# Kernel tuning notes

Measured on AMD Instinct MI355X. Metric: run time of the kernel, lower is better.

The kernel has to match this reference:

```python
import jax, jax.numpy as jnp
import numpy as np

HID = 128  # hidden_channel
C = 256    # feat_channel

def conv1x1(x, w, b):
    # x: [N, Cin, H, W], w: [Cout, Cin], b: [Cout]
    return jnp.einsum('nchw,oc->nohw', x, w) + b[None, :, None, None]

def maxpool2(x):
    N, Ch, H, W = x.shape
    return x.reshape(N, Ch, H // 2, 2, W // 2, 2).max(axis=(3, 5))

def setup_inputs() -> dict:
    key = jax.random.key(0)
    ks = jax.random.split(key, 6)
    rois = jax.random.normal(ks[0], (128, C, 14, 14), dtype=jnp.float32)
    feature = jax.random.normal(ks[1], (2, C, 64, 64), dtype=jnp.float32)
    s_in = 1.0 / np.sqrt(C)
    s_hid = 1.0 / np.sqrt(HID)
    wq = jax.random.uniform(ks[2], (HID, C), minval=-s_in, maxval=s_in, dtype=jnp.float32)
    wk = jax.random.uniform(ks[3], (HID, C), minval=-s_in, maxval=s_in, dtype=jnp.float32)
    wv = jax.random.uniform(ks[4], (HID, C), minval=-s_in, maxval=s_in, dtype=jnp.float32)
    wre = jax.random.uniform(ks[5], (C, HID), minval=-s_hid, maxval=s_hid, dtype=jnp.float32)
    return {
        'rois': rois, 'feature': feature,
        'wq': wq, 'bq': jnp.zeros((HID,), jnp.float32),
        'wk': wk, 'bk': jnp.zeros((HID,), jnp.float32),
        'wv': wv, 'bv': jnp.zeros((HID,), jnp.float32),
        'wre': wre, 'bre': jnp.zeros((C,), jnp.float32),
    }

def reference(rois, feature, wq, bq, wk, bk, wv, bv, wre, bre):
    BS_roinum, Cf, h, w = rois.shape
    BS = feature.shape[0]
    roinum = BS_roinum // BS
    _h, _w = h // 2, w // 2

    # Q at full resolution
    q = conv1x1(rois, wq, bq)                              # [BS*R, HID, h, w]
    q = q.transpose(0, 2, 3, 1).reshape(BS, roinum * h * w, HID)

    ds = maxpool2(rois)                                    # [BS*R, C, _h, _w]
    k = conv1x1(ds, wk, bk).transpose(0, 2, 3, 1).reshape(BS, roinum * _h * _w, HID)
    v = conv1x1(ds, wv, bv).transpose(0, 2, 3, 1).reshape(BS, roinum * _h * _w, HID)

    score = jnp.einsum('bqc,bkc->bqk', q, k)               # [BS, R*h*w, R*_h*_w]
    score = jax.nn.softmax(score, axis=-1)
    y = jnp.einsum('bqk,bkc->bqc', score, v)               # [BS, R*h*w, HID]

    y = y.reshape(BS * roinum, h, w, HID).transpose(0, 3, 1, 2)
    y = conv1x1(y, wre, bre)                               # [BS*R, C, h, w]
    return rois + y
```

## Files before the change

### kernel.cpp

```cpp
#include <hip/hip_runtime.h>
#include <math.h>

constexpr int CIN  = 256;
constexpr int HID  = 128;
constexpr int P    = 196;
constexpr int PP   = 49;
constexpr int NQ   = 12544;
constexpr int NKEY = 3136;

using f32x4 = __attribute__((ext_vector_type(4))) float;
using s16x8 = __attribute__((ext_vector_type(8))) short;
using s16x4 = __attribute__((ext_vector_type(4))) short;
using u32x2 = __attribute__((ext_vector_type(2))) unsigned int;

__device__ __forceinline__ unsigned short f2bf(float x) {
    unsigned int u = __float_as_uint(x);
    u += 0x7FFFu + ((u >> 16) & 1u);
    return (unsigned short)(u >> 16);
}
__device__ __forceinline__ float bf2f(unsigned short s) {
    return __uint_as_float(((unsigned int)s) << 16);
}

__global__ __launch_bounds__(256) void prep_kernel(
    const float* __restrict__ rois,
    const float* __restrict__ wq, const float* __restrict__ wk,
    const float* __restrict__ wv, const float* __restrict__ wre,
    unsigned short* __restrict__ xq, unsigned short* __restrict__ xkv,
    unsigned short* __restrict__ wqb, unsigned short* __restrict__ wkb,
    unsigned short* __restrict__ wvb, unsigned short* __restrict__ wreb)
{
    const int bx = blockIdx.x;
    const int t  = threadIdx.x;

    if (bx >= 512) {
        const int which = bx - 512;
        const float* src = (which == 0) ? wq : (which == 1) ? wk : (which == 2) ? wv : wre;
        unsigned short* dst = (which == 0) ? wqb : (which == 1) ? wkb
                             : (which == 2) ? wvb : wreb;
        #pragma unroll 4
        for (int i = 0; i < 32; ++i) {
            const int idx = i * 256 + t;
            const float4 v = ((const float4*)src)[idx];
            s16x4 o;
            o[0] = (short)f2bf(v.x); o[1] = (short)f2bf(v.y);
            o[2] = (short)f2bf(v.z); o[3] = (short)f2bf(v.w);
            *(s16x4*)(dst + idx * 4) = o;
        }
        return;
    }

    const int n = bx >> 2;
    const int g = bx & 3;
    const int b = n >> 6, r = n & 63;
    __shared__ float xT[196 * 68];

    const int c_loc = t >> 2;
    const int pq    = t & 3;

    const float4* row4 = (const float4*)(rois + ((size_t)n * CIN + g * 64 + c_loc) * P);
    #pragma unroll
    for (int j = 0; j < 13; ++j) {
        const int idx4 = pq + 4 * j;
        if (idx4 < 49) {
            const float4 v = row4[idx4];
            xT[(idx4 * 4 + 0) * 68 + c_loc] = v.x;
            xT[(idx4 * 4 + 1) * 68 + c_loc] = v.y;
            xT[(idx4 * 4 + 2) * 68 + c_loc] = v.z;
            xT[(idx4 * 4 + 3) * 68 + c_loc] = v.w;
        }
    }
    __syncthreads();

    #pragma unroll
    for (int i = 0; i < 7; ++i) {
        const int u = i * 256 + t;
        if (u < 1568) {
            const int px = u >> 3, ch8 = (u & 7) * 8;
            s16x8 o;
            #pragma unroll
            for (int e = 0; e < 8; ++e)
                o[e] = (short)f2bf(xT[px * 68 + ch8 + e]);
            *(s16x8*)(xq + ((size_t)b * NQ + r * P + px) * CIN + g * 64 + ch8) = o;
        }
    }
    #pragma unroll
    for (int i = 0; i < 2; ++i) {
        const int u = i * 256 + t;
        if (u < 392) {
            const int pp = u >> 3, ch8 = (u & 7) * 8;
            const int py = pp / 7, px_ = pp - py * 7;
            const int base00 = (py * 2) * 14 + px_ * 2;
            s16x8 o;
            #pragma unroll
            for (int e = 0; e < 8; ++e) {
                const int c = ch8 + e;
                const float m0 = fmaxf(xT[(base00)      * 68 + c], xT[(base00 + 1)  * 68 + c]);
                const float m1 = fmaxf(xT[(base00 + 14) * 68 + c], xT[(base00 + 15) * 68 + c]);
                o[e] = (short)f2bf(fmaxf(m0, m1));
            }
            *(s16x8*)(xkv + ((size_t)b * NKEY + r * PP + pp) * CIN + g * 64 + ch8) = o;
        }
    }
}

__global__ __launch_bounds__(256) void gemm_fused_kernel(
    const unsigned short* __restrict__ xq, const unsigned short* __restrict__ xkv,
    const unsigned short* __restrict__ wqb, const unsigned short* __restrict__ wkb,
    const unsigned short* __restrict__ wvb,
    const float* __restrict__ bq, const float* __restrict__ bk, const float* __restrict__ bv,
    unsigned short* __restrict__ q, unsigned short* __restrict__ kmat,
    unsigned short* __restrict__ vt_g)
{
    const int bx = blockIdx.x;
    const unsigned short* x; const unsigned short* w; const float* bias;
    int m_blk, mode;
    if (bx < 196)      { mode = 0; x = xq;  w = wqb; bias = bq; m_blk = bx; }
    else if (bx < 245) { mode = 1; x = xkv; w = wkb; bias = bk; m_blk = bx - 196; }
    else               { mode = 2; x = xkv; w = wvb; bias = bv; m_blk = bx - 245; }

    const int t = threadIdx.x;
    const int wid = t >> 6, lane = t & 63;
    const int quad = lane >> 4, c = lane & 15;
    const int m_base = m_blk * 128 + (wid & 1) * 64;
    const int n_base = (wid >> 1) * 64;

    f32x4 acc[4][4];
    #pragma unroll
    for (int i = 0; i < 4; ++i)
        #pragma unroll
        for (int j = 0; j < 4; ++j) acc[i][j] = (f32x4)(0.f);

    #pragma unroll
    for (int ks = 0; ks < 8; ++ks) {
        s16x8 af[4], bf[4];
        #pragma unroll
        for (int mt = 0; mt < 4; ++mt)
            af[mt] = *(const s16x8*)(x + (size_t)(m_base + mt * 16 + c) * CIN + ks * 32 + quad * 8);
        #pragma unroll
        for (int nt = 0; nt < 4; ++nt)
            bf[nt] = *(const s16x8*)(w + (size_t)(n_base + nt * 16 + c) * CIN + ks * 32 + quad * 8);
        #pragma unroll
        for (int mt = 0; mt < 4; ++mt)
            #pragma unroll
            for (int nt = 0; nt < 4; ++nt)
                acc[mt][nt] = __builtin_amdgcn_mfma_f32_16x16x32_bf16(af[mt], bf[nt], acc[mt][nt], 0, 0, 0);
    }

    if (mode <= 1) {
        unsigned short* out = (mode == 0) ? q : kmat;
        #pragma unroll
        for (int nt = 0; nt < 4; ++nt) {
            const float bv_ = bias[n_base + nt * 16 + c];
            #pragma unroll
            for (int mt = 0; mt < 4; ++mt)
                #pragma unroll
                for (int rr = 0; rr < 4; ++rr) {
                    const int m = m_base + mt * 16 + quad * 4 + rr;
                    out[(size_t)m * HID + n_base + nt * 16 + c] = f2bf(acc[mt][nt][rr] + bv_);
                }
        }
    } else {
        #pragma unroll
        for (int nt = 0; nt < 4; ++nt) {
            const int d = n_base + nt * 16 + c;
            const float bv_ = bias[d];
            #pragma unroll
            for (int mt = 0; mt < 4; ++mt)
                #pragma unroll
                for (int rr = 0; rr < 4; ++rr) {
                    const int key_g = m_base + mt * 16 + quad * 4 + rr;
                    const int bb = (key_g >= NKEY) ? 1 : 0;
                    const int kl = key_g - bb * NKEY;
                    vt_g[((size_t)bb * HID + d) * NKEY + kl] = f2bf(acc[mt][nt][rr] + bv_);
                }
        }
    }
}

__global__ __launch_bounds__(128, 2) void attn_kernel(
    const unsigned short* __restrict__ q, const unsigned short* __restrict__ kmat,
    const unsigned short* __restrict__ vt_g,
    unsigned short* __restrict__ opart, float* __restrict__ lpart)
{
    const int b    = blockIdx.y;
    const int s    = blockIdx.z;
    const int tid  = threadIdx.x;
    const int w    = tid >> 6;
    const int lane = tid & 63;
    const int quad = lane >> 4;
    const int c    = lane & 15;
    const int qb   = blockIdx.x * 128 + w * 64;

    __shared__ unsigned short Ps[2][64 * 72];

    const unsigned short* qg = q    + (size_t)b * NQ   * HID;
    const unsigned short* kg = kmat + (size_t)b * NKEY * HID;
    const unsigned short* vt = vt_g + (size_t)b * HID  * NKEY;

    s16x8 qf[4][4];
    #pragma unroll
    for (int nt = 0; nt < 4; ++nt)
        #pragma unroll
        for (int ks = 0; ks < 4; ++ks)
            qf[nt][ks] = *(const s16x8*)(qg + (size_t)(qb + nt * 16 + c) * HID + ks * 32 + quad * 8);

    f32x4 Ob[4][8];
    #pragma unroll
    for (int nt = 0; nt < 4; ++nt)
        #pragma unroll
        for (int nd = 0; nd < 8; ++nd) Ob[nt][nd] = (f32x4)(0.f);
    float l[4] = {0.f, 0.f, 0.f, 0.f};

    const int B6[6] = {0, 20, 40, 60, 79, 98};
    const int kt0 = B6[s], kt1 = B6[s + 1];

    for (int kt = kt0; kt < kt1; ++kt) {
        const int kb = kt * 32;

        f32x4 st[2][4];
        #pragma unroll
        for (int mt = 0; mt < 2; ++mt)
            #pragma unroll
            for (int nt = 0; nt < 4; ++nt) st[mt][nt] = (f32x4)(0.f);
        #pragma unroll
        for (int mt = 0; mt < 2; ++mt) {
            s16x8 kf[4];
            #pragma unroll
            for (int ks = 0; ks < 4; ++ks)
                kf[ks] = *(const s16x8*)(kg + (size_t)(kb + mt * 16 + c) * HID + ks * 32 + quad * 8);
            #pragma unroll
            for (int ks = 0; ks < 4; ++ks)
                #pragma unroll
                for (int nt = 0; nt < 4; ++nt)
                    st[mt][nt] = __builtin_amdgcn_mfma_f32_16x16x32_bf16(kf[ks], qf[nt][ks], st[mt][nt], 0, 0, 0);
        }

        #pragma unroll
        for (int mt = 0; mt < 2; ++mt) {
            #pragma unroll
            for (int nt = 0; nt < 4; ++nt) {
                const float e0 = __expf(st[mt][nt][0]);
                const float e1 = __expf(st[mt][nt][1]);
                const float e2 = __expf(st[mt][nt][2]);
                const float e3 = __expf(st[mt][nt][3]);
                l[nt] += (e0 + e1) + (e2 + e3);
                u32x2 pk;
                pk[0] = (unsigned int)f2bf(e0) | ((unsigned int)f2bf(e1) << 16);
                pk[1] = (unsigned int)f2bf(e2) | ((unsigned int)f2bf(e3) << 16);
                *(u32x2*)&Ps[w][(nt * 16 + c) * 72 + mt * 16 + quad * 4] = pk;
            }
        }

        s16x8 pf[4];
        #pragma unroll
        for (int nt = 0; nt < 4; ++nt)
            pf[nt] = *(const s16x8*)&Ps[w][(nt * 16 + c) * 72 + quad * 8];
        #pragma unroll
        for (int g2 = 0; g2 < 2; ++g2) {
            s16x8 vf[4];
            #pragma unroll
            for (int dd = 0; dd < 4; ++dd)
                vf[dd] = *(const s16x8*)(vt + (size_t)((g2 * 4 + dd) * 16 + c) * NKEY + kb + quad * 8);
            #pragma unroll
            for (int dd = 0; dd < 4; ++dd)
                #pragma unroll
                for (int nt = 0; nt < 4; ++nt)
                    Ob[nt][g2 * 4 + dd] = __builtin_amdgcn_mfma_f32_16x16x32_bf16(pf[nt], vf[dd], Ob[nt][g2 * 4 + dd], 0, 0, 0);
        }
    }

    unsigned short* Op = opart + (size_t)(s * 2 + b) * NQ * HID;
    #pragma unroll
    for (int nt = 0; nt < 4; ++nt) {
        #pragma unroll
        for (int nd = 0; nd < 8; ++nd) {
            #pragma unroll
            for (int rr = 0; rr < 4; ++rr) {
                const int qrow = qb + nt * 16 + quad * 4 + rr;
                Op[(size_t)qrow * HID + nd * 16 + c] = f2bf(Ob[nt][nd][rr]);
            }
        }
    }
    #pragma unroll
    for (int nt = 0; nt < 4; ++nt) {
        l[nt] += __shfl_xor(l[nt], 16, 64);
        l[nt] += __shfl_xor(l[nt], 32, 64);
    }
    if (quad == 0) {
        float* lp = lpart + (size_t)(s * 2 + b) * NQ;
        #pragma unroll
        for (int nt = 0; nt < 4; ++nt) lp[qb + nt * 16 + c] = l[nt];
    }
}

__global__ __launch_bounds__(256) void outproj_kernel(
    const float* __restrict__ rois,
    const unsigned short* __restrict__ opart, const float* __restrict__ lpart,
    const unsigned short* __restrict__ wreb, const float* __restrict__ bre,
    float* __restrict__ out)
{
    const int t = threadIdx.x;
    const int wid = t >> 6, lane = t & 63;
    const int quad = lane >> 4, c = lane & 15;
    const int m0 = blockIdx.x * 64;
    const int b  = (m0 >= NQ) ? 1 : 0;

    __shared__ unsigned short ys[64 * 136];

    {
        const int m_loc = t >> 2, kq = t & 3;
        const int q_local = (m0 + m_loc) - b * NQ;
        float lsum = 0.f;
        #pragma unroll
        for (int sl = 0; sl < 5; ++sl)
            lsum += lpart[(size_t)(sl * 2 + b) * NQ + q_local];
        const float invl = 1.0f / lsum;
        #pragma unroll
        for (int ch = 0; ch < 4; ++ch) {
            float a8[8] = {0, 0, 0, 0, 0, 0, 0, 0};
            #pragma unroll
            for (int sl = 0; sl < 5; ++sl) {
                const s16x8 v = *(const s16x8*)&opart[
                    ((size_t)(sl * 2 + b) * NQ + q_local) * HID + kq * 32 + ch * 8];
                #pragma unroll
                for (int e = 0; e < 8; ++e) a8[e] += bf2f((unsigned short)v[e]);
            }
            s16x8 o;
            #pragma unroll
            for (int e = 0; e < 8; ++e) o[e] = (short)f2bf(a8[e] * invl);
            *(s16x8*)&ys[m_loc * 136 + kq * 32 + ch * 8] = o;
        }
    }
    __syncthreads();

    const int o_base = wid * 64;
    s16x8 af[4][4];
    #pragma unroll
    for (int mt = 0; mt < 4; ++mt)
        #pragma unroll
        for (int ks = 0; ks < 4; ++ks)
            af[mt][ks] = *(const s16x8*)(wreb + (size_t)(o_base + mt * 16 + c) * HID + ks * 32 + quad * 8);

    f32x4 acc[4][4];
    #pragma unroll
    for (int i = 0; i < 4; ++i)
        #pragma unroll
        for (int j = 0; j < 4; ++j) acc[i][j] = (f32x4)(0.f);

    #pragma unroll
    for (int ks = 0; ks < 4; ++ks) {
        s16x8 bf[4];
        #pragma unroll
        for (int nt = 0; nt < 4; ++nt)
            bf[nt] = *(const s16x8*)&ys[(nt * 16 + c) * 136 + ks * 32 + quad * 8];
        #pragma unroll
        for (int mt = 0; mt < 4; ++mt)
            #pragma unroll
            for (int nt = 0; nt < 4; ++nt)
                acc[mt][nt] = __builtin_amdgcn_mfma_f32_16x16x32_bf16(af[mt][ks], bf[nt], acc[mt][nt], 0, 0, 0);
    }

    #pragma unroll
    for (int nt = 0; nt < 4; ++nt) {
        const int m_g = m0 + nt * 16 + c;
        const int mm  = m_g - b * NQ;
        const int r_roi = mm / 196;
        const int p     = mm - r_roi * 196;
        const int n_img = b * 64 + r_roi;
        const size_t base = ((size_t)n_img * CIN) * P + p;
        #pragma unroll
        for (int mt = 0; mt < 4; ++mt) {
            #pragma unroll
            for (int rr = 0; rr < 4; ++rr) {
                const int o = o_base + mt * 16 + quad * 4 + rr;
                out[base + (size_t)o * P] = rois[base + (size_t)o * P] + bre[o] + acc[mt][nt][rr];
            }
        }
    }
}

extern "C" void kernel_launch(void* const* d_in, const int* in_sizes, int n_in,
                              void* d_out, int out_size, void* d_ws, size_t ws_size,
                              hipStream_t stream)
{
    (void)in_sizes; (void)n_in; (void)out_size; (void)ws_size;
    const float* rois = (const float*)d_in[0];
    const float* wq  = (const float*)d_in[2];
    const float* bq  = (const float*)d_in[3];
    const float* wk  = (const float*)d_in[4];
    const float* bk  = (const float*)d_in[5];
    const float* wv  = (const float*)d_in[6];
    const float* bv  = (const float*)d_in[7];
    const float* wre = (const float*)d_in[8];
    const float* bre = (const float*)d_in[9];
    float* out = (float*)d_out;

    char* ws = (char*)d_ws;
    unsigned short* opart = (unsigned short*)(ws);
    unsigned short* xq    = (unsigned short*)(ws);
    unsigned short* xkv   = (unsigned short*)(ws + 12845056);
    unsigned short* wqb   = (unsigned short*)(ws + 16056320);
    unsigned short* wkb   = (unsigned short*)(ws + 16121856);
    unsigned short* wvb   = (unsigned short*)(ws + 16187392);
    unsigned short* q     = (unsigned short*)(ws + 32112640);
    unsigned short* kmat  = (unsigned short*)(ws + 38535168);
    unsigned short* vt_g  = (unsigned short*)(ws + 40140800);
    float*          lpart = (float*)         (ws + 41746432);
    unsigned short* wreb  = (unsigned short*)(ws + 42248192);

    prep_kernel<<<dim3(516), 256, 0, stream>>>(rois, wq, wk, wv, wre,
                                               xq, xkv, wqb, wkb, wvb, wreb);
    gemm_fused_kernel<<<dim3(294), 256, 0, stream>>>(xq, xkv, wqb, wkb, wvb,
                                                     bq, bk, bv, q, kmat, vt_g);
    attn_kernel<<<dim3(98, 2, 5), 128, 0, stream>>>(q, kmat, vt_g, opart, lpart);
    outproj_kernel<<<dim3(392), 256, 0, stream>>>(rois, opart, lpart, wreb, bre, out);
}
```

Baseline: 230.1 us.

## Make attention key-split count depend on workspace size; use cheaper bf16 packing

Attention split count S over the key dimension now depends on the available workspace (10, 8 or 5), which raises the grid size and the occupancy of the attention kernel. The workspace layout is recomputed so each split gets its own partial-output buffer, and the reduce loop in outproj is generalized to S. Separately, the bf16 conversion changes from round-to-nearest-even to a simpler round-half-up and packs pairs with v_perm, so it uses fewer instructions. The trade-off is more partial-sum traffic in the reduce, and slightly different rounding.

Result: slower. 240.4 us (+4.5%).

```diff
diff --git a/kernel.cpp b/kernel.cpp
--- a/kernel.cpp
+++ b/kernel.cpp
@@ -12,11 +12,15 @@
 using s16x8 = __attribute__((ext_vector_type(8))) short;
 using s16x4 = __attribute__((ext_vector_type(4))) short;
 using u32x2 = __attribute__((ext_vector_type(2))) unsigned int;
+using u32x4 = __attribute__((ext_vector_type(4))) unsigned int;
 
 __device__ __forceinline__ unsigned short f2bf(float x) {
-    unsigned int u = __float_as_uint(x);
-    u += 0x7FFFu + ((u >> 16) & 1u);
-    return (unsigned short)(u >> 16);
+    return (unsigned short)((__float_as_uint(x) + 0x8000u) >> 16);
+}
+__device__ __forceinline__ unsigned int pack_bf16(float a, float b) {
+    const unsigned int ua = __float_as_uint(a) + 0x8000u;
+    const unsigned int ub = __float_as_uint(b) + 0x8000u;
+    return __builtin_amdgcn_perm(ua, ub, 0x03020706u);
 }
 __device__ __forceinline__ float bf2f(unsigned short s) {
     return __uint_as_float(((unsigned int)s) << 16);
@@ -42,10 +46,10 @@
         for (int i = 0; i < 32; ++i) {
             const int idx = i * 256 + t;
             const float4 v = ((const float4*)src)[idx];
-            s16x4 o;
-            o[0] = (short)f2bf(v.x); o[1] = (short)f2bf(v.y);
-            o[2] = (short)f2bf(v.z); o[3] = (short)f2bf(v.w);
-            *(s16x4*)(dst + idx * 4) = o;
+            u32x2 o;
+            o[0] = pack_bf16(v.x, v.y);
+            o[1] = pack_bf16(v.z, v.w);
+            *(u32x2*)(dst + idx * 4) = o;
         }
         return;
     }
@@ -77,11 +81,11 @@
         const int u = i * 256 + t;
         if (u < 1568) {
             const int px = u >> 3, ch8 = (u & 7) * 8;
-            s16x8 o;
-            #pragma unroll
-            for (int e = 0; e < 8; ++e)
-                o[e] = (short)f2bf(xT[px * 68 + ch8 + e]);
-            *(s16x8*)(xq + ((size_t)b * NQ + r * P + px) * CIN + g * 64 + ch8) = o;
+            u32x4 o;
+            #pragma unroll
+            for (int e = 0; e < 4; ++e)
+                o[e] = pack_bf16(xT[px * 68 + ch8 + 2 * e], xT[px * 68 + ch8 + 2 * e + 1]);
+            *(u32x4*)(xq + ((size_t)b * NQ + r * P + px) * CIN + g * 64 + ch8) = o;
         }
     }
     #pragma unroll
@@ -91,15 +95,18 @@
             const int pp = u >> 3, ch8 = (u & 7) * 8;
             const int py = pp / 7, px_ = pp - py * 7;
             const int base00 = (py * 2) * 14 + px_ * 2;
-            s16x8 o;
+            float mx[8];
             #pragma unroll
             for (int e = 0; e < 8; ++e) {
                 const int c = ch8 + e;
                 const float m0 = fmaxf(xT[(base00)      * 68 + c], xT[(base00 + 1)  * 68 + c]);
                 const float m1 = fmaxf(xT[(base00 + 14) * 68 + c], xT[(base00 + 15) * 68 + c]);
-                o[e] = (short)f2bf(fmaxf(m0, m1));
+                mx[e] = fmaxf(m0, m1);
             }
-            *(s16x8*)(xkv + ((size_t)b * NKEY + r * PP + pp) * CIN + g * 64 + ch8) = o;
+            u32x4 o;
+            #pragma unroll
+            for (int e = 0; e < 4; ++e) o[e] = pack_bf16(mx[2 * e], mx[2 * e + 1]);
+            *(u32x4*)(xkv + ((size_t)b * NKEY + r * PP + pp) * CIN + g * 64 + ch8) = o;
         }
     }
 }
@@ -181,7 +188,7 @@
 __global__ __launch_bounds__(128, 2) void attn_kernel(
     const unsigned short* __restrict__ q, const unsigned short* __restrict__ kmat,
     const unsigned short* __restrict__ vt_g,
-    unsigned short* __restrict__ opart, float* __restrict__ lpart)
+    unsigned short* __restrict__ opart, float* __restrict__ lpart, int S)
 {
     const int b    = blockIdx.y;
     const int s    = blockIdx.z;
@@ -212,8 +219,8 @@
         for (int nd = 0; nd < 8; ++nd) Ob[nt][nd] = (f32x4)(0.f);
     float l[4] = {0.f, 0.f, 0.f, 0.f};
 
-    const int B6[6] = {0, 20, 40, 60, 79, 98};
-    const int kt0 = B6[s], kt1 = B6[s + 1];
+    const int kt0 = (98 * s) / S;
+    const int kt1 = (98 * (s + 1)) / S;
 
     for (int kt = kt0; kt < kt1; ++kt) {
         const int kb = kt * 32;
@@ -246,8 +253,8 @@
                 const float e3 = __expf(st[mt][nt][3]);
                 l[nt] += (e0 + e1) + (e2 + e3);
                 u32x2 pk;
-                pk[0] = (unsigned int)f2bf(e0) | ((unsigned int)f2bf(e1) << 16);
-                pk[1] = (unsigned int)f2bf(e2) | ((unsigned int)f2bf(e3) << 16);
+                pk[0] = pack_bf16(e0, e1);
+                pk[1] = pack_bf16(e2, e3);
                 *(u32x2*)&Ps[w][(nt * 16 + c) * 72 + mt * 16 + quad * 4] = pk;
             }
         }
@@ -298,7 +305,7 @@
     const float* __restrict__ rois,
     const unsigned short* __restrict__ opart, const float* __restrict__ lpart,
     const unsigned short* __restrict__ wreb, const float* __restrict__ bre,
-    float* __restrict__ out)
+    float* __restrict__ out, int S)
 {
     const int t = threadIdx.x;
     const int wid = t >> 6, lane = t & 63;
@@ -312,24 +319,28 @@
         const int m_loc = t >> 2, kq = t & 3;
         const int q_local = (m0 + m_loc) - b * NQ;
         float lsum = 0.f;
-        #pragma unroll
-        for (int sl = 0; sl < 5; ++sl)
+        for (int sl = 0; sl < S; ++sl)
             lsum += lpart[(size_t)(sl * 2 + b) * NQ + q_local];
         const float invl = 1.0f / lsum;
-        #pragma unroll
-        for (int ch = 0; ch < 4; ++ch) {
-            float a8[8] = {0, 0, 0, 0, 0, 0, 0, 0};
-            #pragma unroll
-            for (int sl = 0; sl < 5; ++sl) {
+        float a32[32];
+        #pragma unroll
+        for (int e = 0; e < 32; ++e) a32[e] = 0.f;
+        for (int sl = 0; sl < S; ++sl) {
+            #pragma unroll
+            for (int ch = 0; ch < 4; ++ch) {
                 const s16x8 v = *(const s16x8*)&opart[
                     ((size_t)(sl * 2 + b) * NQ + q_local) * HID + kq * 32 + ch * 8];
                 #pragma unroll
-                for (int e = 0; e < 8; ++e) a8[e] += bf2f((unsigned short)v[e]);
+                for (int e = 0; e < 8; ++e) a32[ch * 8 + e] += bf2f((unsigned short)v[e]);
             }
-            s16x8 o;
-            #pragma unroll
-            for (int e = 0; e < 8; ++e) o[e] = (short)f2bf(a8[e] * invl);
-            *(s16x8*)&ys[m_loc * 136 + kq * 32 + ch * 8] = o;
+        }
+        #pragma unroll
+        for (int ch = 0; ch < 4; ++ch) {
+            u32x4 o;
+            #pragma unroll
+            for (int e = 0; e < 4; ++e)
+                o[e] = pack_bf16(a32[ch * 8 + 2 * e] * invl, a32[ch * 8 + 2 * e + 1] * invl);
+            *(u32x4*)&ys[m_loc * 136 + kq * 32 + ch * 8] = o;
         }
     }
     __syncthreads();
@@ -384,7 +395,7 @@
                               void* d_out, int out_size, void* d_ws, size_t ws_size,
                               hipStream_t stream)
 {
-    (void)in_sizes; (void)n_in; (void)out_size; (void)ws_size;
+    (void)in_sizes; (void)n_in; (void)out_size;
     const float* rois = (const float*)d_in[0];
     const float* wq  = (const float*)d_in[2];
     const float* bq  = (const float*)d_in[3];
@@ -396,23 +407,28 @@
     const float* bre = (const float*)d_in[9];
     float* out = (float*)d_out;
 
+    int S = (ws_size >= (size_t)74928128) ? 10
+          : (ws_size >= (size_t)61882368) ? 8 : 5;
+
     char* ws = (char*)d_ws;
+    const size_t opart_bytes = (size_t)2 * S * 3211264;
     unsigned short* opart = (unsigned short*)(ws);
     unsigned short* xq    = (unsigned short*)(ws);
     unsigned short* xkv   = (unsigned short*)(ws + 12845056);
     unsigned short* wqb   = (unsigned short*)(ws + 16056320);
     unsigned short* wkb   = (unsigned short*)(ws + 16121856);
     unsigned short* wvb   = (unsigned short*)(ws + 16187392);
-    unsigned short* q     = (unsigned short*)(ws + 32112640);
-    unsigned short* kmat  = (unsigned short*)(ws + 38535168);
-    unsigned short* vt_g  = (unsigned short*)(ws + 40140800);
-    float*          lpart = (float*)         (ws + 41746432);
-    unsigned short* wreb  = (unsigned short*)(ws + 42248192);
+    char* p = ws + opart_bytes;
+    unsigned short* q     = (unsigned short*)(p);
+    unsigned short* kmat  = (unsigned short*)(p + 6422528);
+    unsigned short* vt_g  = (unsigned short*)(p + 8028160);
+    float*          lpart = (float*)         (p + 9633792);
+    unsigned short* wreb  = (unsigned short*)(p + 9633792 + (size_t)2 * S * 50176);
 
     prep_kernel<<<dim3(516), 256, 0, stream>>>(rois, wq, wk, wv, wre,
                                                xq, xkv, wqb, wkb, wvb, wreb);
     gemm_fused_kernel<<<dim3(294), 256, 0, stream>>>(xq, xkv, wqb, wkb, wvb,
                                                      bq, bk, bv, q, kmat, vt_g);
-    attn_kernel<<<dim3(98, 2, 5), 128, 0, stream>>>(q, kmat, vt_g, opart, lpart);
-    outproj_kernel<<<dim3(392), 256, 0, stream>>>(rois, opart, lpart, wreb, bre, out);
-}
+    attn_kernel<<<dim3(98, 2, S), 128, 0, stream>>>(q, kmat, vt_g, opart, lpart, S);
+    outproj_kernel<<<dim3(392), 256, 0, stream>>>(rois, opart, lpart, wreb, bre, out, S);
+}
```
